# Performance work log

Measured on AMD Instinct MI355X. Metric: run time of the kernel, lower is better.

The kernel has to match this reference:

```python
import jax, jax.numpy as jnp
import numpy as np
import math

HIDDEN = 1024
HEADS = 16
HEAD_DIM = HIDDEN // HEADS


def setup_inputs() -> dict:
    key = jax.random.key(0)
    ks = jax.random.split(key, 9)
    s = 1.0 / math.sqrt(HIDDEN)
    x = jax.random.normal(ks[0], (4, 2048, HIDDEN), dtype=jnp.float32)
    Wq = jax.random.uniform(ks[1], (HIDDEN, HIDDEN), jnp.float32, -s, s)
    bq = jax.random.uniform(ks[2], (HIDDEN,), jnp.float32, -s, s)
    Wk = jax.random.uniform(ks[3], (HIDDEN, HIDDEN), jnp.float32, -s, s)
    bk = jax.random.uniform(ks[4], (HIDDEN,), jnp.float32, -s, s)
    Wv = jax.random.uniform(ks[5], (HIDDEN, HIDDEN), jnp.float32, -s, s)
    bv = jax.random.uniform(ks[6], (HIDDEN,), jnp.float32, -s, s)
    Wo = jax.random.uniform(ks[7], (HIDDEN, HIDDEN), jnp.float32, -s, s)
    bo = jax.random.uniform(ks[8], (HIDDEN,), jnp.float32, -s, s)
    return {"x": x, "Wq": Wq, "bq": bq, "Wk": Wk, "bk": bk,
            "Wv": Wv, "bv": bv, "Wo": Wo, "bo": bo}


def reference(x, Wq, bq, Wk, bk, Wv, bv, Wo, bo):
    B, T, D = x.shape
    H, Hd = HEADS, HEAD_DIM
    scale = 1.0 / math.sqrt(Hd)
    # projections (torch Linear: y = x @ W.T + b)
    q = (x @ Wq.T + bq).reshape(B, T, H, Hd).transpose(0, 2, 1, 3)  # [B,H,T,Hd]
    k = (x @ Wk.T + bk).reshape(B, T, H, Hd).transpose(0, 2, 1, 3)
    v = (x @ Wv.T + bv).reshape(B, T, H, Hd).transpose(0, 2, 1, 3)
    scores = jnp.einsum("bhqd,bhkd->bhqk", q, k) * scale  # [B,H,T,T]
    attn = jax.nn.softmax(scores, axis=-1)
    out = jnp.einsum("bhqk,bhkd->bhqd", attn, v)  # [B,H,T,Hd]
    out = out.transpose(0, 2, 1, 3).reshape(B, T, D)
    out = out @ Wo.T + bo
    return out.mean(axis=1)  # [B, D]
```

## Files before the change

kernel.cpp:

```cpp
#include <hip/hip_runtime.h>
#include <stdint.h>

#define HIDDEN 1024
#define HEADS 16
#define HEAD_DIM 64
#define BATCH 4
#define SEQ 2048
#define NTOK (BATCH * SEQ)

typedef __attribute__((ext_vector_type(8))) short bf16x8;
typedef __attribute__((ext_vector_type(4))) float floatx4;
typedef __attribute__((ext_vector_type(16))) float floatx16;

#define SCALE_Q 0.18033688011112042f

__device__ __forceinline__ unsigned short f2bf(float f) {
    union { float f; unsigned u; } x; x.f = f;
    unsigned r = x.u + 0x7fffu + ((x.u >> 16) & 1u);
    return (unsigned short)(r >> 16);
}

__device__ __forceinline__ float fast_exp2(float x) {
#if __has_builtin(__builtin_amdgcn_exp2f)
    return __builtin_amdgcn_exp2f(x);
#else
    return exp2f(x);
#endif
}

typedef __attribute__((address_space(3))) unsigned int lds_u32;
typedef const __attribute__((address_space(1))) unsigned int gl_u32;

__device__ __forceinline__ void async_cp16(const void* g, void* l) {
#if __has_builtin(__builtin_amdgcn_global_load_lds)
    __builtin_amdgcn_global_load_lds((gl_u32*)g, (lds_u32*)l, 16, 0, 0);
#else
    *(uint4*)((char*)l + (threadIdx.x & 63) * 16) = *(const uint4*)g;
#endif
}

__global__ __launch_bounds__(256) void conv_all(
    const float* __restrict__ x, const float* __restrict__ Wq,
    const float* __restrict__ Wk, const float* __restrict__ Wv,
    unsigned short* __restrict__ x_bf, unsigned short* __restrict__ wq_bf,
    unsigned short* __restrict__ wk_bf, unsigned short* __restrict__ wv_bf,
    float* __restrict__ accp) {
    const int blk = blockIdx.x, tid = threadIdx.x;
    const float* src;
    unsigned short* dst;
    size_t i;
    if (blk < 8192) {
        src = x; dst = x_bf; i = (size_t)blk * 256 + tid;
        if (blk < 16) accp[blk * 256 + tid] = 0.0f;
    } else {
        int r = blk - 8192;
        int s = r >> 10;
        src = (s == 0) ? Wq : (s == 1) ? Wk : Wv;
        dst = (s == 0) ? wq_bf : (s == 1) ? wk_bf : wv_bf;
        i = (size_t)(r & 1023) * 256 + tid;
    }
    float4 v = *(const float4*)(src + 4 * i);
    unsigned short o[4];
    o[0] = f2bf(v.x); o[1] = f2bf(v.y); o[2] = f2bf(v.z); o[3] = f2bf(v.w);
    *(ushort4*)(dst + 4 * i) = *(ushort4*)o;
}

__global__ __launch_bounds__(256, 3) void qkv_gemm(
    const unsigned short* __restrict__ X,
    const unsigned short* __restrict__ W0, const unsigned short* __restrict__ W1,
    const unsigned short* __restrict__ W2,
    const float* __restrict__ b0, const float* __restrict__ b1,
    const float* __restrict__ b2,
    unsigned short* __restrict__ O0, unsigned short* __restrict__ O1,
    unsigned short* __restrict__ O2) {
    __shared__ __align__(16) char smem[49152];
    unsigned short* tbuf = (unsigned short*)smem;

    const int id = blockIdx.x;
    const int mb = id & 63, nzb = id >> 6;
    const int z = nzb >> 3, nz = nzb & 7;
    const int m0 = mb * 128;
    const unsigned short* W = (z == 0) ? W0 : (z == 1) ? W1 : W2;
    const float* bias       = (z == 0) ? b0 : (z == 1) ? b1 : b2;

    const int tid = threadIdx.x, lane = tid & 63, wave = tid >> 6;
    const int wm = (wave & 1) * 64, wn = (wave >> 1) * 64;

    const int srow = lane >> 2;
    const int sxc = ((lane & 3) ^ (srow & 3)) * 8;
    const unsigned short* ga[2];
    const unsigned short* gb[2];
#pragma unroll
    for (int j = 0; j < 2; ++j) {
        ga[j] = X + (size_t)(m0 + wave * 32 + j * 16 + srow) * HIDDEN + sxc;
        gb[j] = W + (size_t)(nz * 128 + wave * 32 + j * 16 + srow) * HIDDEN + sxc;
    }

    floatx4 acc[4][4];
#pragma unroll
    for (int tm = 0; tm < 4; ++tm)
#pragma unroll
        for (int tn = 0; tn < 4; ++tn)
#pragma unroll
            for (int r = 0; r < 4; ++r) acc[tm][tn][r] = 0.f;

    auto STAGE = [&](int s) {
#pragma unroll
        for (int j = 0; j < 2; ++j) {
            async_cp16(ga[j], smem + s * 16384 + wave * 2048 + j * 1024);
            async_cp16(gb[j], smem + s * 16384 + 8192 + wave * 2048 + j * 1024);
            ga[j] += 32; gb[j] += 32;
        }
    };
    const int fr = (lane & 15) * 64 + (((lane >> 4) ^ (lane & 3)) * 16);
    auto COMPUTE = [&](int s) {
        const char* Ab = smem + s * 16384;
        const char* Bb = Ab + 8192;
        bf16x8 af[4], bfr[4];
#pragma unroll
        for (int t = 0; t < 4; ++t) {
            af[t]  = *(bf16x8*)(Ab + (wm + t * 16) * 64 + fr);
            bfr[t] = *(bf16x8*)(Bb + (wn + t * 16) * 64 + fr);
        }
        __builtin_amdgcn_s_setprio(1);
#pragma unroll
        for (int tm = 0; tm < 4; ++tm)
#pragma unroll
            for (int tn = 0; tn < 4; ++tn)
                acc[tm][tn] = __builtin_amdgcn_mfma_f32_16x16x32_bf16(af[tm], bfr[tn], acc[tm][tn], 0, 0, 0);
        __builtin_amdgcn_s_setprio(0);
    };

    STAGE(0);
    STAGE(1);

    int rs = 0, ss = 2;
    for (int kt = 0; kt < 30; ++kt) {
        STAGE(ss);
        asm volatile("s_waitcnt vmcnt(8)" ::: "memory");
        __builtin_amdgcn_sched_barrier(0);
        asm volatile("s_barrier" ::: "memory");
        __builtin_amdgcn_sched_barrier(0);
        COMPUTE(rs);
        asm volatile("s_waitcnt lgkmcnt(0)" ::: "memory");
        __builtin_amdgcn_sched_barrier(0);
        asm volatile("s_barrier" ::: "memory");
        __builtin_amdgcn_sched_barrier(0);
        rs = (rs == 2) ? 0 : rs + 1;
        ss = (ss == 2) ? 0 : ss + 1;
    }
    asm volatile("s_waitcnt vmcnt(4)" ::: "memory");
    __builtin_amdgcn_sched_barrier(0);
    asm volatile("s_barrier" ::: "memory");
    __builtin_amdgcn_sched_barrier(0);
    COMPUTE(rs);
    asm volatile("s_waitcnt lgkmcnt(0)" ::: "memory");
    __builtin_amdgcn_sched_barrier(0);
    asm volatile("s_barrier" ::: "memory");
    __builtin_amdgcn_sched_barrier(0);
    rs = (rs == 2) ? 0 : rs + 1;
    asm volatile("s_waitcnt vmcnt(0)" ::: "memory");
    __builtin_amdgcn_sched_barrier(0);
    asm volatile("s_barrier" ::: "memory");
    __builtin_amdgcn_sched_barrier(0);
    COMPUTE(rs);

    const int col = lane & 15, rbase = (lane >> 4) * 4;
    __syncthreads();
    if (z == 2) {
#pragma unroll
        for (int tm = 0; tm < 4; ++tm)
#pragma unroll
            for (int tn = 0; tn < 4; ++tn) {
                const int dr = wn + tn * 16 + col;
                const float bs = bias[nz * 128 + dr];
                const int mi0 = wm + tm * 16 + rbase;
                const int mip = (mi0 & ~12) | ((mi0 & 4) << 1) | ((mi0 & 8) >> 1);
                unsigned short vals[4];
#pragma unroll
                for (int r = 0; r < 4; ++r) vals[r] = f2bf(acc[tm][tn][r] + bs);
                *(ushort4*)&tbuf[dr * 136 + mip] = *(ushort4*)vals;
            }
        __syncthreads();
        const int dr = tid >> 1, seg = tid & 1;
        const int hh = nz * 2 + (dr >> 6), dd = dr & 63;
        const int bb = m0 >> 11, tb = (m0 & (SEQ - 1)) >> 7;
        unsigned short* dst = O2 + (((size_t)bb * HEADS + hh) * HEAD_DIM + dd) * SEQ
                                 + tb * 128 + seg * 64;
        const unsigned short* srcl = &tbuf[dr * 136 + seg * 64];
#pragma unroll
        for (int i = 0; i < 8; ++i)
            *(uint4*)(dst + i * 8) = *(const uint4*)(srcl + i * 8);
    } else {
        unsigned short* O = (z == 0) ? O0 : O1;
        const float sc = (z == 0) ? SCALE_Q : 1.0f;
#pragma unroll
        for (int tm = 0; tm < 4; ++tm)
#pragma unroll
            for (int tn = 0; tn < 4; ++tn) {
                const int nn = wn + tn * 16 + col;
                const float bs = bias[nz * 128 + nn];
                const int mi0 = wm + tm * 16 + rbase;
#pragma unroll
                for (int r = 0; r < 4; ++r)
                    tbuf[(mi0 + r) * 136 + nn] = f2bf((acc[tm][tn][r] + bs) * sc);
            }
        __syncthreads();
        const int r = tid >> 1, seg = tid & 1;
        unsigned short* dst = O + (size_t)(m0 + r) * HIDDEN + nz * 128 + seg * 64;
        const unsigned short* srcl = &tbuf[r * 136 + seg * 64];
#pragma unroll
        for (int i = 0; i < 8; ++i)
            *(uint4*)(dst + i * 8) = *(const uint4*)(srcl + i * 8);
    }
}

__global__ __launch_bounds__(128, 2) void attn_mfma(
    const unsigned short* __restrict__ Q, const unsigned short* __restrict__ K,
    const unsigned short* __restrict__ Vt, float* __restrict__ accp) {
    __shared__ unsigned short Klds[2][4096];
    __shared__ unsigned short Vlds[2][4096];

    const int tid = threadIdx.x, lane = tid & 63, wave = tid >> 6;
    const int lq = lane & 31, g2 = lane >> 5;

    const int f = blockIdx.x;
    const int bh = (f & 7) * 8 + ((f >> 3) & 7);
    const int qc = f >> 6;
    const int b = bh >> 4, h = bh & 15;

    bf16x8 qfrag[2][4];
#pragma unroll
    for (int grp = 0; grp < 2; ++grp) {
        const size_t qb = ((size_t)(b * SEQ + qc * 128 + wave * 64 + grp * 32 + lq)) * HIDDEN
                          + h * HEAD_DIM + g2 * 8;
#pragma unroll
        for (int ds = 0; ds < 4; ++ds) qfrag[grp][ds] = *(const bf16x8*)&Q[qb + ds * 16];
    }

    const unsigned short* kg[4];
    const unsigned short* vg[4];
    {
        const int kr = lane >> 3;
        const int kc = ((lane & 7) ^ kr) * 8;
#pragma unroll
        for (int j = 0; j < 4; ++j)
            kg[j] = K + ((size_t)(b * SEQ + wave * 32 + j * 8 + kr)) * HIDDEN + h * HEAD_DIM + kc;
#pragma unroll
        for (int j = 0; j < 4; ++j) {
            const int dl = wave * 32 + j * 8 + (lane >> 3);
            const int cc = ((lane & 7) ^ (dl & 7)) * 8;
            vg[j] = Vt + ((size_t)bh * HEAD_DIM + dl) * SEQ + cc;
        }
    }

    floatx16 oacc[2][2];
#pragma unroll
    for (int r = 0; r < 16; ++r) {
        oacc[0][0][r] = 0.f; oacc[0][1][r] = 0.f;
        oacc[1][0][r] = 0.f; oacc[1][1][r] = 0.f;
    }
    float lsum00 = 0.f, lsum01 = 0.f, lsum10 = 0.f, lsum11 = 0.f;

#pragma unroll
    for (int j = 0; j < 4; ++j) {
        async_cp16(kg[j], (char*)Klds[0] + (wave * 32 + j * 8) * 128);
        async_cp16(vg[j], (char*)Vlds[0] + (wave * 32 + j * 8) * 128);
        kg[j] += 64 * HIDDEN; vg[j] += 64;
    }
    __syncthreads();

    for (int it = 0; it < 32; ++it) {
        const int cur = it & 1;
        if (it < 31) {
#pragma unroll
            for (int j = 0; j < 4; ++j) {
                async_cp16(kg[j], (char*)Klds[cur ^ 1] + (wave * 32 + j * 8) * 128);
                async_cp16(vg[j], (char*)Vlds[cur ^ 1] + (wave * 32 + j * 8) * 128);
                kg[j] += 64 * HIDDEN; vg[j] += 64;
            }
        }
#pragma unroll
        for (int s32 = 0; s32 < 2; ++s32) {
            const int rr = s32 * 32 + lq;
            bf16x8 kf[4];
#pragma unroll
            for (int ds = 0; ds < 4; ++ds)
                kf[ds] = *(bf16x8*)((char*)Klds[cur] + rr * 128 + (((g2 + 2 * ds) ^ (lq & 7)) * 16));

            floatx16 sacc0, sacc1;
#pragma unroll
            for (int r = 0; r < 16; ++r) { sacc0[r] = 0.f; sacc1[r] = 0.f; }
#pragma unroll
            for (int ds = 0; ds < 4; ++ds)
                sacc0 = __builtin_amdgcn_mfma_f32_32x32x16_bf16(kf[ds], qfrag[0][ds], sacc0, 0, 0, 0);
#pragma unroll
            for (int ds = 0; ds < 4; ++ds)
                sacc1 = __builtin_amdgcn_mfma_f32_32x32x16_bf16(kf[ds], qfrag[1][ds], sacc1, 0, 0, 0);

            bf16x8 vf[2][2];
#pragma unroll
            for (int ks2 = 0; ks2 < 2; ++ks2)
#pragma unroll
                for (int nf = 0; nf < 2; ++nf) {
                    const int d = nf * 32 + lq;
                    const int c = (2 * (s32 * 2 + ks2) + g2) ^ (d & 7);
                    vf[ks2][nf] = *(bf16x8*)((char*)Vlds[cur] + d * 128 + c * 16);
                }

            unsigned pk[2][8];
#pragma unroll
            for (int j = 0; j < 8; ++j) {
                union { float f; unsigned u; } plo, phi;
                plo.f = fast_exp2(sacc0[2 * j]);
                phi.f = fast_exp2(sacc0[2 * j + 1]);
                lsum00 += plo.f; lsum01 += phi.f;
                pk[0][j] = __builtin_amdgcn_perm(phi.u, plo.u, 0x07060302u);
            }
#pragma unroll
            for (int j = 0; j < 8; ++j) {
                union { float f; unsigned u; } plo, phi;
                plo.f = fast_exp2(sacc1[2 * j]);
                phi.f = fast_exp2(sacc1[2 * j + 1]);
                lsum10 += plo.f; lsum11 += phi.f;
                pk[1][j] = __builtin_amdgcn_perm(phi.u, plo.u, 0x07060302u);
            }

#pragma unroll
            for (int ks2 = 0; ks2 < 2; ++ks2)
#pragma unroll
                for (int grp = 0; grp < 2; ++grp) {
                    union { uint4 u; bf16x8 v; } af;
                    af.u.x = pk[grp][4 * ks2];
                    af.u.y = pk[grp][4 * ks2 + 1];
                    af.u.z = pk[grp][4 * ks2 + 2];
                    af.u.w = pk[grp][4 * ks2 + 3];
#pragma unroll
                    for (int nf = 0; nf < 2; ++nf)
                        oacc[grp][nf] = __builtin_amdgcn_mfma_f32_32x32x16_bf16(af.v, vf[ks2][nf], oacc[grp][nf], 0, 0, 0);
                }
        }
        if (it < 31) __syncthreads();
    }

    float linv[2][16];
#pragma unroll
    for (int grp = 0; grp < 2; ++grp) {
        float lf = (grp == 0) ? (lsum00 + lsum01) : (lsum10 + lsum11);
        lf += __shfl_xor(lf, 32, 64);
#pragma unroll
        for (int r = 0; r < 16; ++r) {
            const int qr = (r & 3) + 8 * (r >> 2) + 4 * g2;
            linv[grp][r] = 1.0f / __shfl(lf, qr, 64);
        }
    }
#pragma unroll
    for (int nf = 0; nf < 2; ++nf) {
        float v = 0.f;
#pragma unroll
        for (int r = 0; r < 16; ++r)
            v += oacc[0][nf][r] * linv[0][r] + oacc[1][nf][r] * linv[1][r];
        v += __shfl_xor(v, 32, 64);
        if (lane < 32)
            atomicAdd(&accp[b * HIDDEN + h * HEAD_DIM + nf * 32 + lq], v);
    }
}

__global__ __launch_bounds__(256) void out_proj(const float* __restrict__ acc,
                                                const float* __restrict__ Wo,
                                                const float* __restrict__ bo,
                                                float* __restrict__ out) {
    const int tid = threadIdx.x;
    const int nl = tid >> 6, lane = tid & 63;
    const int n = blockIdx.x * 4 + nl;
    const float* wr = Wo + (size_t)n * HIDDEN + lane * 16;
    float s0 = 0.f, s1 = 0.f, s2 = 0.f, s3 = 0.f;
#pragma unroll
    for (int kk = 0; kk < 4; ++kk) {
        float4 w = *(const float4*)(wr + kk * 4);
        float4 a0 = *(const float4*)(acc + 0 * HIDDEN + lane * 16 + kk * 4);
        float4 a1 = *(const float4*)(acc + 1 * HIDDEN + lane * 16 + kk * 4);
        float4 a2 = *(const float4*)(acc + 2 * HIDDEN + lane * 16 + kk * 4);
        float4 a3 = *(const float4*)(acc + 3 * HIDDEN + lane * 16 + kk * 4);
        s0 += w.x * a0.x + w.y * a0.y + w.z * a0.z + w.w * a0.w;
        s1 += w.x * a1.x + w.y * a1.y + w.z * a1.z + w.w * a1.w;
        s2 += w.x * a2.x + w.y * a2.y + w.z * a2.z + w.w * a2.w;
        s3 += w.x * a3.x + w.y * a3.y + w.z * a3.z + w.w * a3.w;
    }
#pragma unroll
    for (int off = 32; off; off >>= 1) {
        s0 += __shfl_xor(s0, off, 64);
        s1 += __shfl_xor(s1, off, 64);
        s2 += __shfl_xor(s2, off, 64);
        s3 += __shfl_xor(s3, off, 64);
    }
    if (lane < 4) {
        float sv = (lane == 0) ? s0 : (lane == 1) ? s1 : (lane == 2) ? s2 : s3;
        out[lane * HIDDEN + n] = sv * (1.0f / (float)SEQ) + bo[n];
    }
}

extern "C" void kernel_launch(void* const* d_in, const int* in_sizes, int n_in,
                              void* d_out, int out_size, void* d_ws, size_t ws_size,
                              hipStream_t stream) {
    const float* x  = (const float*)d_in[0];
    const float* Wq = (const float*)d_in[1];
    const float* bq = (const float*)d_in[2];
    const float* Wk = (const float*)d_in[3];
    const float* bk = (const float*)d_in[4];
    const float* Wv = (const float*)d_in[5];
    const float* bv = (const float*)d_in[6];
    const float* Wo = (const float*)d_in[7];
    const float* bo = (const float*)d_in[8];
    float* out = (float*)d_out;

    char* ws = (char*)d_ws;
    unsigned short* x_bf  = (unsigned short*)(ws);
    unsigned short* wq_bf = (unsigned short*)(ws + 16777216);
    unsigned short* wk_bf = (unsigned short*)(ws + 18874368);
    unsigned short* wv_bf = (unsigned short*)(ws + 20971520);
    unsigned short* q_bf  = (unsigned short*)(ws + 23068672);
    unsigned short* k_bf  = (unsigned short*)(ws + 39845888);
    unsigned short* vt_bf = (unsigned short*)(ws + 56623104);
    float*          accp  = (float*)(ws + 73400320);

    conv_all<<<dim3(8192 + 3072), dim3(256), 0, stream>>>(
        x, Wq, Wk, Wv, x_bf, wq_bf, wk_bf, wv_bf, accp);

    qkv_gemm<<<dim3(1536), dim3(256), 0, stream>>>(
        x_bf, wq_bf, wk_bf, wv_bf, bq, bk, bv, q_bf, k_bf, vt_bf);

    attn_mfma<<<dim3(1024), dim3(128), 0, stream>>>(q_bf, k_bf, vt_bf, accp);

    out_proj<<<dim3(256), dim3(256), 0, stream>>>(accp, Wo, bo, out);
}
```

Measured before the change: 234.7 us.

## Enlarge QKV GEMM tile to 256x128 with double buffering

The QKV projection GEMM now computes a 256x128 output tile per block instead of 128x128. Each wave holds 8x4 MFMA accumulators, which improves the operand reuse of the weight tile and halves the grid. The LDS pipeline drops from three stages to two, since each stage is now larger, and the epilogue writes the two 128-row halves in sequence through the shared transpose buffer. Occupancy falls from 3 to 2 blocks per CU, and the shallower prefetch gives less room to hide latency.

```diff
diff --git a/kernel.cpp b/kernel.cpp
--- a/kernel.cpp
+++ b/kernel.cpp
@@ -65,7 +65,7 @@
     *(ushort4*)(dst + 4 * i) = *(ushort4*)o;
 }
 
-__global__ __launch_bounds__(256, 3) void qkv_gemm(
+__global__ __launch_bounds__(256, 2) void qkv_gemm(
     const unsigned short* __restrict__ X,
     const unsigned short* __restrict__ W0, const unsigned short* __restrict__ W1,
     const unsigned short* __restrict__ W2,
@@ -77,28 +77,30 @@
     unsigned short* tbuf = (unsigned short*)smem;
 
     const int id = blockIdx.x;
-    const int mb = id & 63, nzb = id >> 6;
+    const int mb = id & 31, nzb = id >> 5;
     const int z = nzb >> 3, nz = nzb & 7;
-    const int m0 = mb * 128;
+    const int m0 = mb * 256;
     const unsigned short* W = (z == 0) ? W0 : (z == 1) ? W1 : W2;
     const float* bias       = (z == 0) ? b0 : (z == 1) ? b1 : b2;
 
     const int tid = threadIdx.x, lane = tid & 63, wave = tid >> 6;
-    const int wm = (wave & 1) * 64, wn = (wave >> 1) * 64;
+    const int wmB = (wave & 1) * 128;
+    const int wn  = (wave >> 1) * 64;
 
     const int srow = lane >> 2;
     const int sxc = ((lane & 3) ^ (srow & 3)) * 8;
-    const unsigned short* ga[2];
+    const unsigned short* ga[4];
     const unsigned short* gb[2];
 #pragma unroll
-    for (int j = 0; j < 2; ++j) {
-        ga[j] = X + (size_t)(m0 + wave * 32 + j * 16 + srow) * HIDDEN + sxc;
+    for (int j = 0; j < 4; ++j)
+        ga[j] = X + (size_t)(m0 + wave * 64 + j * 16 + srow) * HIDDEN + sxc;
+#pragma unroll
+    for (int j = 0; j < 2; ++j)
         gb[j] = W + (size_t)(nz * 128 + wave * 32 + j * 16 + srow) * HIDDEN + sxc;
-    }
-
-    floatx4 acc[4][4];
-#pragma unroll
-    for (int tm = 0; tm < 4; ++tm)
+
+    floatx4 acc[8][4];
+#pragma unroll
+    for (int tm = 0; tm < 8; ++tm)
 #pragma unroll
         for (int tn = 0; tn < 4; ++tn)
 #pragma unroll
@@ -106,25 +108,30 @@
 
     auto STAGE = [&](int s) {
 #pragma unroll
+        for (int j = 0; j < 4; ++j) {
+            async_cp16(ga[j], smem + s * 24576 + wave * 4096 + j * 1024);
+            ga[j] += 32;
+        }
+#pragma unroll
         for (int j = 0; j < 2; ++j) {
-            async_cp16(ga[j], smem + s * 16384 + wave * 2048 + j * 1024);
-            async_cp16(gb[j], smem + s * 16384 + 8192 + wave * 2048 + j * 1024);
-            ga[j] += 32; gb[j] += 32;
+            async_cp16(gb[j], smem + s * 24576 + 16384 + wave * 2048 + j * 1024);
+            gb[j] += 32;
         }
     };
     const int fr = (lane & 15) * 64 + (((lane >> 4) ^ (lane & 3)) * 16);
     auto COMPUTE = [&](int s) {
-        const char* Ab = smem + s * 16384;
-        const char* Bb = Ab + 8192;
-        bf16x8 af[4], bfr[4];
-#pragma unroll
-        for (int t = 0; t < 4; ++t) {
-            af[t]  = *(bf16x8*)(Ab + (wm + t * 16) * 64 + fr);
+        const char* Ab = smem + s * 24576;
+        const char* Bb = Ab + 16384;
+        bf16x8 af[8], bfr[4];
+#pragma unroll
+        for (int t = 0; t < 8; ++t)
+            af[t]  = *(bf16x8*)(Ab + (wmB + t * 16) * 64 + fr);
+#pragma unroll
+        for (int t = 0; t < 4; ++t)
             bfr[t] = *(bf16x8*)(Bb + (wn + t * 16) * 64 + fr);
-        }
         __builtin_amdgcn_s_setprio(1);
 #pragma unroll
-        for (int tm = 0; tm < 4; ++tm)
+        for (int tm = 0; tm < 8; ++tm)
 #pragma unroll
             for (int tn = 0; tn < 4; ++tn)
                 acc[tm][tn] = __builtin_amdgcn_mfma_f32_16x16x32_bf16(af[tm], bfr[tn], acc[tm][tn], 0, 0, 0);
@@ -132,86 +139,83 @@
     };
 
     STAGE(0);
-    STAGE(1);
-
-    int rs = 0, ss = 2;
-    for (int kt = 0; kt < 30; ++kt) {
-        STAGE(ss);
-        asm volatile("s_waitcnt vmcnt(8)" ::: "memory");
+
+    int cur = 0;
+    for (int kt = 0; kt < 31; ++kt) {
+        STAGE(cur ^ 1);
+        asm volatile("s_waitcnt vmcnt(6)" ::: "memory");
         __builtin_amdgcn_sched_barrier(0);
         asm volatile("s_barrier" ::: "memory");
         __builtin_amdgcn_sched_barrier(0);
-        COMPUTE(rs);
+        COMPUTE(cur);
         asm volatile("s_waitcnt lgkmcnt(0)" ::: "memory");
         __builtin_amdgcn_sched_barrier(0);
         asm volatile("s_barrier" ::: "memory");
         __builtin_amdgcn_sched_barrier(0);
-        rs = (rs == 2) ? 0 : rs + 1;
-        ss = (ss == 2) ? 0 : ss + 1;
-    }
-    asm volatile("s_waitcnt vmcnt(4)" ::: "memory");
-    __builtin_amdgcn_sched_barrier(0);
-    asm volatile("s_barrier" ::: "memory");
-    __builtin_amdgcn_sched_barrier(0);
-    COMPUTE(rs);
-    asm volatile("s_waitcnt lgkmcnt(0)" ::: "memory");
-    __builtin_amdgcn_sched_barrier(0);
-    asm volatile("s_barrier" ::: "memory");
-    __builtin_amdgcn_sched_barrier(0);
-    rs = (rs == 2) ? 0 : rs + 1;
+        cur ^= 1;
+    }
     asm volatile("s_waitcnt vmcnt(0)" ::: "memory");
     __builtin_amdgcn_sched_barrier(0);
     asm volatile("s_barrier" ::: "memory");
     __builtin_amdgcn_sched_barrier(0);
-    COMPUTE(rs);
+    COMPUTE(cur);
 
     const int col = lane & 15, rbase = (lane >> 4) * 4;
     __syncthreads();
-    if (z == 2) {
-#pragma unroll
-        for (int tm = 0; tm < 4; ++tm)
-#pragma unroll
-            for (int tn = 0; tn < 4; ++tn) {
-                const int dr = wn + tn * 16 + col;
-                const float bs = bias[nz * 128 + dr];
-                const int mi0 = wm + tm * 16 + rbase;
-                const int mip = (mi0 & ~12) | ((mi0 & 4) << 1) | ((mi0 & 8) >> 1);
-                unsigned short vals[4];
-#pragma unroll
-                for (int r = 0; r < 4; ++r) vals[r] = f2bf(acc[tm][tn][r] + bs);
-                *(ushort4*)&tbuf[dr * 136 + mip] = *(ushort4*)vals;
+#pragma unroll
+    for (int p = 0; p < 2; ++p) {
+        if ((wave & 1) == p) {
+            if (z == 2) {
+#pragma unroll
+                for (int tm = 0; tm < 8; ++tm)
+#pragma unroll
+                    for (int tn = 0; tn < 4; ++tn) {
+                        const int dr = wn + tn * 16 + col;
+                        const float bs = bias[nz * 128 + dr];
+                        const int mi0 = tm * 16 + rbase;
+                        const int mip = (mi0 & ~12) | ((mi0 & 4) << 1) | ((mi0 & 8) >> 1);
+                        unsigned short vals[4];
+#pragma unroll
+                        for (int r = 0; r < 4; ++r) vals[r] = f2bf(acc[tm][tn][r] + bs);
+                        *(ushort4*)&tbuf[dr * 136 + mip] = *(ushort4*)vals;
+                    }
+            } else {
+                const float sc = (z == 0) ? SCALE_Q : 1.0f;
+#pragma unroll
+                for (int tm = 0; tm < 8; ++tm)
+#pragma unroll
+                    for (int tn = 0; tn < 4; ++tn) {
+                        const int nn = wn + tn * 16 + col;
+                        const float bs = bias[nz * 128 + nn];
+                        const int mi0 = tm * 16 + rbase;
+#pragma unroll
+                        for (int r = 0; r < 4; ++r)
+                            tbuf[(mi0 + r) * 136 + nn] = f2bf((acc[tm][tn][r] + bs) * sc);
+                    }
             }
+        }
         __syncthreads();
-        const int dr = tid >> 1, seg = tid & 1;
-        const int hh = nz * 2 + (dr >> 6), dd = dr & 63;
-        const int bb = m0 >> 11, tb = (m0 & (SEQ - 1)) >> 7;
-        unsigned short* dst = O2 + (((size_t)bb * HEADS + hh) * HEAD_DIM + dd) * SEQ
-                                 + tb * 128 + seg * 64;
-        const unsigned short* srcl = &tbuf[dr * 136 + seg * 64];
-#pragma unroll
-        for (int i = 0; i < 8; ++i)
-            *(uint4*)(dst + i * 8) = *(const uint4*)(srcl + i * 8);
-    } else {
-        unsigned short* O = (z == 0) ? O0 : O1;
-        const float sc = (z == 0) ? SCALE_Q : 1.0f;
-#pragma unroll
-        for (int tm = 0; tm < 4; ++tm)
-#pragma unroll
-            for (int tn = 0; tn < 4; ++tn) {
-                const int nn = wn + tn * 16 + col;
-                const float bs = bias[nz * 128 + nn];
-                const int mi0 = wm + tm * 16 + rbase;
-#pragma unroll
-                for (int r = 0; r < 4; ++r)
-                    tbuf[(mi0 + r) * 136 + nn] = f2bf((acc[tm][tn][r] + bs) * sc);
-            }
+        if (z == 2) {
+            const int dr = tid >> 1, seg = tid & 1;
+            const int hh = nz * 2 + (dr >> 6), dd = dr & 63;
+            const int mrow = m0 + p * 128;
+            const int bb = mrow >> 11, tb = (mrow & (SEQ - 1)) >> 7;
+            unsigned short* dst = O2 + (((size_t)bb * HEADS + hh) * HEAD_DIM + dd) * SEQ
+                                     + tb * 128 + seg * 64;
+            const unsigned short* srcl = &tbuf[dr * 136 + seg * 64];
+#pragma unroll
+            for (int i = 0; i < 8; ++i)
+                *(uint4*)(dst + i * 8) = *(const uint4*)(srcl + i * 8);
+        } else {
+            unsigned short* O = (z == 0) ? O0 : O1;
+            const int r = tid >> 1, seg = tid & 1;
+            unsigned short* dst = O + (size_t)(m0 + p * 128 + r) * HIDDEN + nz * 128 + seg * 64;
+            const unsigned short* srcl = &tbuf[r * 136 + seg * 64];
+#pragma unroll
+            for (int i = 0; i < 8; ++i)
+                *(uint4*)(dst + i * 8) = *(const uint4*)(srcl + i * 8);
+        }
         __syncthreads();
-        const int r = tid >> 1, seg = tid & 1;
-        unsigned short* dst = O + (size_t)(m0 + r) * HIDDEN + nz * 128 + seg * 64;
-        const unsigned short* srcl = &tbuf[r * 136 + seg * 64];
-#pragma unroll
-        for (int i = 0; i < 8; ++i)
-            *(uint4*)(dst + i * 8) = *(const uint4*)(srcl + i * 8);
     }
 }
 
@@ -427,7 +431,7 @@
     conv_all<<<dim3(8192 + 3072), dim3(256), 0, stream>>>(
         x, Wq, Wk, Wv, x_bf, wq_bf, wk_bf, wv_bf, accp);
 
-    qkv_gemm<<<dim3(1536), dim3(256), 0, stream>>>(
+    qkv_gemm<<<dim3(768), dim3(256), 0, stream>>>(
         x_bf, wq_bf, wk_bf, wv_bf, bq, bk, bv, q_bf, k_bf, vt_bf);
 
     attn_mfma<<<dim3(1024), dim3(128), 0, stream>>>(q_bf, k_bf, vt_bf, accp);
```

Result: slower. 244.5 us (+4.2%).
